# Kernel optimization log

Measured on AMD Instinct MI355X. Metric: run time of the kernel, lower is better.

Reference implementation:

```python
import jax, jax.numpy as jnp
import numpy as np

N, C = 16384, 1000
P, Q, EPS = 0.6, 1.5, 0.01

def setup_inputs() -> dict:
    key = jax.random.key(0)
    k1, k2, k3 = jax.random.split(key, 3)
    logits = jax.random.normal(k1, (N, C), dtype=jnp.float32)
    targets = jax.random.randint(k2, (N,), 0, C, dtype=jnp.int64)
    # long-tailed cumulative class counts (float buffer in the torch module)
    cum_counts = jax.random.randint(k3, (C,), 1, 100000).astype(jnp.float32)
    return {"logits": logits, "targets": targets, "cum_counts": cum_counts}

def reference(logits, targets, cum_counts):
    # Seesaw loss (eval mode: no count update), reduction='mean'.
    n = logits.shape[0]
    tgt_count = jnp.maximum(cum_counts[targets], 1.0)            # (N,)  clamped target-class count
    # Mitigation factor: (count_j / count_t + eps)^p where count_j < count_t (strict)
    ratio_c = cum_counts[None, :] / tgt_count[:, None]           # (N, C)
    mitigation = jnp.where(cum_counts[None, :] < tgt_count[:, None],
                           jnp.power(ratio_c + EPS, P), 1.0)
    # Compensation factor: (p_j / (p_t + eps))^q where p_j > p_t
    probs = jax.nn.softmax(logits, axis=1)                       # (N, C)
    tgt_prob = jnp.take_along_axis(probs, targets[:, None], axis=1)  # (N, 1)
    compensation = jnp.where(probs > tgt_prob,
                             jnp.power(probs / (tgt_prob + EPS), Q), 1.0)
    # j == target column is always weight 1 (loops skip it)
    onehot = jax.nn.one_hot(targets, logits.shape[1], dtype=bool)
    weights = jnp.where(onehot, 1.0, mitigation * compensation)  # (N, C)
    weighted_logits = logits + jnp.log(weights + EPS)
    logp = jax.nn.log_softmax(weighted_logits, axis=1)
    loss = -jnp.take_along_axis(logp, targets[:, None], axis=1)[:, 0]
    return jnp.mean(loss)
```

## Files before the change

kernel.cpp:

```cpp
#include <hip/hip_runtime.h>
#include <math.h>


#define SSL_N 16384
#define SSL_C 1000
#define SSL_C4 250
#define SSL_P 0.6f
#define SSL_Q 1.5f
#define SSL_EPS 0.01f
#define SSL_LOG1PE 0.00995033085f
#define WPB 4
#define NBLK (SSL_N / WPB)
#define NEG_INF (-INFINITY)

__device__ __forceinline__ float wterm(float l, float c, float ct,
                                       float inv_ct, float lt, float QK) {
    const float lm = (c < ct) ? SSL_P * __logf(fmaf(c, inv_ct, SSL_EPS)) : 0.0f;
    const float lc = (l > lt) ? fmaf(SSL_Q, l, -QK) : 0.0f;
    return __expf(l + lm + lc);
}

__global__ __launch_bounds__(256, 8) void seesaw_main(
    const float* __restrict__ logits,
    const int*   __restrict__ targets,
    const float* __restrict__ cum_counts,
    float*       __restrict__ partial)
{
    __shared__ float cc[1024];

    const int lane = threadIdx.x & 63;
    const int gw   = blockIdx.x * WPB + (threadIdx.x >> 6);

    const int t = targets[gw];

    const float4* __restrict__ lrow4 =
        reinterpret_cast<const float4*>(logits + (size_t)gw * SSL_C);

    const float4 lv0 = lrow4[lane];
    const float4 lv1 = lrow4[lane + 64];
    const float4 lv2 = lrow4[lane + 128];
    const float4 lv3 = (lane + 192 < SSL_C4)
        ? lrow4[lane + 192]
        : make_float4(NEG_INF, NEG_INF, NEG_INF, NEG_INF);

    {
        const float4* __restrict__ cc4p = reinterpret_cast<const float4*>(cum_counts);
        const int i = threadIdx.x;
        const float4 v = (i < SSL_C4) ? cc4p[i] : make_float4(1.0f, 1.0f, 1.0f, 1.0f);
        *reinterpret_cast<float4*>(&cc[4 * i]) = v;
    }
    __syncthreads();

    const int t4 = t >> 2;
    const int cs = t & 3;
    float s1 = 0.0f, lta = 0.0f;

#define SSL_ACC(LVK, K)                                                        \
    {                                                                          \
        s1 += __expf(LVK.x); s1 += __expf(LVK.y);                              \
        s1 += __expf(LVK.z); s1 += __expf(LVK.w);                              \
        const float sel = (cs == 0) ? LVK.x : (cs == 1) ? LVK.y                \
                        : (cs == 2) ? LVK.z : LVK.w;     \
        lta += (lane + 64 * K == t4) ? sel : 0.0f;                             \
    }
    SSL_ACC(lv0, 0) SSL_ACC(lv1, 1) SSL_ACC(lv2, 2) SSL_ACC(lv3, 3)
#undef SSL_ACC

    #pragma unroll
    for (int off = 32; off >= 1; off >>= 1) {
        s1  += __shfl_xor(s1,  off, 64);
        lta += __shfl_xor(lta, off, 64);
    }
    const float lt = lta;

    const float ct     = fmaxf(cc[t], 1.0f);
    const float pt     = __expf(lt) / s1;
    const float QK     = SSL_Q * (__logf(s1) + __logf(pt + SSL_EPS));
    const float inv_ct = 1.0f / ct;

    float s = 0.0f;
#define SSL_PB(LVK, K)                                                         \
    {                                                                          \
        const float4 c4 = *reinterpret_cast<const float4*>(&cc[4 * (lane + 64 * K)]); \
        s += wterm(LVK.x, c4.x, ct, inv_ct, lt, QK);                           \
        s += wterm(LVK.y, c4.y, ct, inv_ct, lt, QK);                           \
        s += wterm(LVK.z, c4.z, ct, inv_ct, lt, QK);                           \
        s += wterm(LVK.w, c4.w, ct, inv_ct, lt, QK);                           \
    }
    SSL_PB(lv0, 0) SSL_PB(lv1, 1) SSL_PB(lv2, 2) SSL_PB(lv3, 3)
#undef SSL_PB

    #pragma unroll
    for (int off = 32; off >= 1; off >>= 1)
        s += __shfl_xor(s, off, 64);

    const float s2 = fmaf(SSL_EPS, s1, s);

    if (lane == 0)
        partial[gw] = __logf(s2) - lt - SSL_LOG1PE;
}

__global__ __launch_bounds__(1024) void ssl_reduce(
    const float* __restrict__ partial, float* __restrict__ out)
{
    const float4* __restrict__ p4 = reinterpret_cast<const float4*>(partial);
    float s = 0.0f;
    #pragma unroll
    for (int k = 0; k < 4; ++k) {
        const float4 v = p4[threadIdx.x + 1024 * k];
        s += (v.x + v.y) + (v.z + v.w);
    }
    #pragma unroll
    for (int off = 32; off >= 1; off >>= 1) s += __shfl_xor(s, off, 64);
    __shared__ float ws[16];
    if ((threadIdx.x & 63) == 0) ws[threadIdx.x >> 6] = s;
    __syncthreads();
    if (threadIdx.x == 0) {
        float a = 0.0f;
        #pragma unroll
        for (int w = 0; w < 16; ++w) a += ws[w];
        out[0] = a * (1.0f / SSL_N);
    }
}

extern "C" void kernel_launch(void* const* d_in, const int* in_sizes, int n_in,
                              void* d_out, int out_size, void* d_ws, size_t ws_size,
                              hipStream_t stream) {
    const float* logits     = (const float*)d_in[0];
    const int*   targets    = (const int*)d_in[1];
    const float* cum_counts = (const float*)d_in[2];
    float* out     = (float*)d_out;
    float* partial = (float*)d_ws;

    seesaw_main<<<NBLK, 256, 0, stream>>>(logits, targets, cum_counts, partial);
    ssl_reduce<<<1, 1024, 0, stream>>>(partial, out);
}
```

Before: 99.49 us.

## Precompute both weighted exponentials before reduction to break serial dependency

The per-element weighted terms are restructured so both candidate exponentials (with and without the compensation factor) are computed in the first pass, before the row max/target reduction completes. The target-dependent QK scale is factored out as a single exp(-QK) multiply applied after the reduction, and the branch condition l>lt becomes a comparison V > U*exp(Q*lt). This removes the dependency of the second pass on the shuffle reduction, but adds one extra exp per element, holds 32 more registers, and risks overflow/precision changes from exp(2.5*l).

```diff
diff --git a/kernel.cpp b/kernel.cpp
--- a/kernel.cpp
+++ b/kernel.cpp
@@ -13,13 +13,6 @@
 #define NBLK (SSL_N / WPB)
 #define NEG_INF (-INFINITY)
 
-__device__ __forceinline__ float wterm(float l, float c, float ct,
-                                       float inv_ct, float lt, float QK) {
-    const float lm = (c < ct) ? SSL_P * __logf(fmaf(c, inv_ct, SSL_EPS)) : 0.0f;
-    const float lc = (l > lt) ? fmaf(SSL_Q, l, -QK) : 0.0f;
-    return __expf(l + lm + lc);
-}
-
 __global__ __launch_bounds__(256, 8) void seesaw_main(
     const float* __restrict__ logits,
     const int*   __restrict__ targets,
@@ -33,9 +26,15 @@
 
     const int t = targets[gw];
 
+    {
+        const float4* __restrict__ cc4p = reinterpret_cast<const float4*>(cum_counts);
+        const int i = threadIdx.x;
+        const float4 v = (i < SSL_C4) ? cc4p[i] : make_float4(1.0f, 1.0f, 1.0f, 1.0f);
+        *reinterpret_cast<float4*>(&cc[4 * i]) = v;
+    }
+
     const float4* __restrict__ lrow4 =
         reinterpret_cast<const float4*>(logits + (size_t)gw * SSL_C);
-
     const float4 lv0 = lrow4[lane];
     const float4 lv1 = lrow4[lane + 64];
     const float4 lv2 = lrow4[lane + 128];
@@ -43,28 +42,40 @@
         ? lrow4[lane + 192]
         : make_float4(NEG_INF, NEG_INF, NEG_INF, NEG_INF);
 
-    {
-        const float4* __restrict__ cc4p = reinterpret_cast<const float4*>(cum_counts);
-        const int i = threadIdx.x;
-        const float4 v = (i < SSL_C4) ? cc4p[i] : make_float4(1.0f, 1.0f, 1.0f, 1.0f);
-        *reinterpret_cast<float4*>(&cc[4 * i]) = v;
-    }
     __syncthreads();
 
-    const int t4 = t >> 2;
-    const int cs = t & 3;
+    const float ct     = fmaxf(cc[t], 1.0f);
+    const float inv_ct = 1.0f / ct;
+    const int   t4     = t >> 2;
+    const int   cs     = t & 3;
+
     float s1 = 0.0f, lta = 0.0f;
+    float4 u0, u1, u2, u3, v0, v1, v2, v3;
 
-#define SSL_ACC(LVK, K)                                                        \
+#define SSL_E(L, CV, OU, OV)                                                   \
     {                                                                          \
-        s1 += __expf(LVK.x); s1 += __expf(LVK.y);                              \
-        s1 += __expf(LVK.z); s1 += __expf(LVK.w);                              \
+        s1 += __expf(L);                                                       \
+        const float lm = (CV < ct) ? SSL_P * __logf(fmaf(CV, inv_ct, SSL_EPS)) \
+                                   : 0.0f;                                     \
+        OU = __expf(L + lm);                              \
+        OV = __expf(fmaf(SSL_Q, L, L + lm));           \
+    }
+#define SSL_CH(LVK, UK, VK, K)                                                 \
+    {                                                                          \
+        const float4 c4 =                                                      \
+            *reinterpret_cast<const float4*>(&cc[4 * (lane + 64 * K)]);        \
+        SSL_E(LVK.x, c4.x, UK.x, VK.x)                                         \
+        SSL_E(LVK.y, c4.y, UK.y, VK.y)                                         \
+        SSL_E(LVK.z, c4.z, UK.z, VK.z)                                         \
+        SSL_E(LVK.w, c4.w, UK.w, VK.w)                                         \
         const float sel = (cs == 0) ? LVK.x : (cs == 1) ? LVK.y                \
                         : (cs == 2) ? LVK.z : LVK.w;     \
         lta += (lane + 64 * K == t4) ? sel : 0.0f;                             \
     }
-    SSL_ACC(lv0, 0) SSL_ACC(lv1, 1) SSL_ACC(lv2, 2) SSL_ACC(lv3, 3)
-#undef SSL_ACC
+    SSL_CH(lv0, u0, v0, 0) SSL_CH(lv1, u1, v1, 1)
+    SSL_CH(lv2, u2, v2, 2) SSL_CH(lv3, u3, v3, 3)
+#undef SSL_CH
+#undef SSL_E
 
     #pragma unroll
     for (int off = 32; off >= 1; off >>= 1) {
@@ -73,28 +84,29 @@
     }
     const float lt = lta;
 
-    const float ct     = fmaxf(cc[t], 1.0f);
-    const float pt     = __expf(lt) / s1;
-    const float QK     = SSL_Q * (__logf(s1) + __logf(pt + SSL_EPS));
-    const float inv_ct = 1.0f / ct;
-
-    float s = 0.0f;
-#define SSL_PB(LVK, K)                                                         \
+    const float eQlt = __expf(SSL_Q * lt);
+    float slo = 0.0f, shi = 0.0f;
+#define SSL_S(U, V)                                                            \
     {                                                                          \
-        const float4 c4 = *reinterpret_cast<const float4*>(&cc[4 * (lane + 64 * K)]); \
-        s += wterm(LVK.x, c4.x, ct, inv_ct, lt, QK);                           \
-        s += wterm(LVK.y, c4.y, ct, inv_ct, lt, QK);                           \
-        s += wterm(LVK.z, c4.z, ct, inv_ct, lt, QK);                           \
-        s += wterm(LVK.w, c4.w, ct, inv_ct, lt, QK);                           \
+        const bool hi = (V > U * eQlt);                                        \
+        slo += hi ? 0.0f : U;                                                  \
+        shi += hi ? V : 0.0f;                                                  \
     }
-    SSL_PB(lv0, 0) SSL_PB(lv1, 1) SSL_PB(lv2, 2) SSL_PB(lv3, 3)
-#undef SSL_PB
+#define SSL_S4(UK, VK) SSL_S(UK.x, VK.x) SSL_S(UK.y, VK.y)                     \
+                       SSL_S(UK.z, VK.z) SSL_S(UK.w, VK.w)
+    SSL_S4(u0, v0) SSL_S4(u1, v1) SSL_S4(u2, v2) SSL_S4(u3, v3)
+#undef SSL_S4
+#undef SSL_S
 
     #pragma unroll
-    for (int off = 32; off >= 1; off >>= 1)
-        s += __shfl_xor(s, off, 64);
+    for (int off = 32; off >= 1; off >>= 1) {
+        slo += __shfl_xor(slo, off, 64);
+        shi += __shfl_xor(shi, off, 64);
+    }
 
-    const float s2 = fmaf(SSL_EPS, s1, s);
+    const float pt = __expf(lt) / s1;
+    const float QK = SSL_Q * (__logf(s1) + __logf(pt + SSL_EPS));
+    const float s2 = fmaf(SSL_EPS, s1, fmaf(shi, __expf(-QK), slo));
 
     if (lane == 0)
         partial[gw] = __logf(s2) - lt - SSL_LOG1PE;
```

Result: slower. 102.0 us (+2.5%).
